# Performance work log

Measured on AMD Instinct MI355X. Metric: run time of the kernel, lower is better.

The kernel has to match this reference:

```python
import jax, jax.numpy as jnp
import numpy as np

IMG_H, IMG_W = 432.0, 768.0
B, N = 8, 1_000_000


def setup_inputs() -> dict:
    key = jax.random.key(0)
    k1, k2 = jax.random.split(key)
    scores = jax.random.uniform(k1, (B, N, 1), dtype=jnp.float32)
    # center-format boxes (x, y, w, h) roughly in image coords so masks fire
    scale = jnp.array([IMG_W, IMG_H, 256.0, 256.0], dtype=jnp.float32)
    rps = jax.random.uniform(k2, (B, N, 4), dtype=jnp.float32) * scale
    return {"scores": scores, "rps": rps, "n_train_pre_nms": 12000}


def _anchors_clip(boxes):
    # boxes: [B, N, 4] in (cx, cy, w, h)
    cx, cy, w, h = boxes[..., 0], boxes[..., 1], boxes[..., 2], boxes[..., 3]
    x1 = jnp.clip(cx - w * 0.5, 0.0, IMG_W)
    x2 = jnp.clip(cx + w * 0.5, 0.0, IMG_W)
    y1 = jnp.clip(cy - h * 0.5, 0.0, IMG_H)
    y2 = jnp.clip(cy + h * 0.5, 0.0, IMG_H)
    nw = x2 - x1
    nh = y2 - y1
    nx = x1 + nw * 0.5
    ny = y1 + nh * 0.5
    return jnp.stack([nx, ny, nw, nh], axis=-1)


def reference(scores, rps, n_train_pre_nms):
    rois = _anchors_clip(rps)                                   # [B, N, 4]
    mask = ((rois[..., 2] > 16.0) & (rois[..., 3] > 16.0))
    s = scores * mask.astype(scores.dtype)[..., None]           # [B, N, 1]
    # full descending argsort along anchor dim, keep top n_train_pre_nms
    order = jnp.argsort(-s[..., 0], axis=1)[:, :n_train_pre_nms]  # [B, K]
    rois_sel = jnp.take_along_axis(rois, order[..., None], axis=1)  # [B, K, 4]
    s_sel = jnp.take_along_axis(s, order[..., None], axis=1)        # [B, K, 1]
    return rois_sel, s_sel
```

## Files before the change

kernel.cpp:

```cpp
#include <hip/hip_runtime.h>
#include <stdint.h>

#define BATCH   8
#define NITEMS  1000000
#define NC      64
#define NF      4096
#define NBLK    128
#define CAP     32768
#define TOPBIN  (NC - 1)
#define IMG_W   768.0f
#define IMG_H   432.0f

static __device__ __forceinline__ float clip0(float v, float hi) {
    return fminf(fmaxf(v, 0.0f), hi);
}
static __device__ __forceinline__ int cbin(float s) {
    int g = (int)(s * (float)NC);
    return g > NC - 1 ? NC - 1 : (g < 0 ? 0 : g);
}
static __device__ __forceinline__ int fbin(float s, int g) {
    int f = (int)(s * (float)(NC * NF)) - g * NF;
    return f > NF - 1 ? NF - 1 : (f < 0 ? 0 : f);
}
static __device__ __forceinline__ unsigned mkbits(float4 box, float s) {
    float x1 = clip0(box.x - box.z * 0.5f, IMG_W);
    float x2 = clip0(box.x + box.z * 0.5f, IMG_W);
    float y1 = clip0(box.y - box.w * 0.5f, IMG_H);
    float y2 = clip0(box.y + box.w * 0.5f, IMG_H);
    bool m = ((x2 - x1) > 16.0f) && ((y2 - y1) > 16.0f);
    return __float_as_uint(m ? s : 0.0f);
}

__global__ __launch_bounds__(512)
void k_bits_hist(const float* __restrict__ scores,
                 const float4* __restrict__ rps,
                 uint4* __restrict__ bits_arr,
                 unsigned short* __restrict__ p1,
                 unsigned short* __restrict__ p2) {
    __shared__ unsigned h1[NC];
    __shared__ unsigned h2[NF];
    const int b = blockIdx.y, blk = blockIdx.x, tid = threadIdx.x;
    if (tid < NC) h1[tid] = 0u;
    for (int k = tid; k < NF; k += 512) h2[k] = 0u;
    __syncthreads();
    const int base = b * NITEMS;
    for (int i0 = (blk * 512 + tid) * 4; i0 < NITEMS; i0 += NBLK * 512 * 4) {
        const float4 sc = *(const float4*)(scores + base + i0);
        const float4 bx0 = rps[base + i0 + 0];
        const float4 bx1 = rps[base + i0 + 1];
        const float4 bx2 = rps[base + i0 + 2];
        const float4 bx3 = rps[base + i0 + 3];
        uint4 ob;
        ob.x = mkbits(bx0, sc.x);
        ob.y = mkbits(bx1, sc.y);
        ob.z = mkbits(bx2, sc.z);
        ob.w = mkbits(bx3, sc.w);
        unsigned arr[4] = {ob.x, ob.y, ob.z, ob.w};
        #pragma unroll
        for (int j = 0; j < 4; j++) {
            unsigned bits = arr[j];
            if (bits) {
                float s = __uint_as_float(bits);
                int g = cbin(s);
                atomicAdd(&h1[g], 1u);
                if (g == TOPBIN) atomicAdd(&h2[fbin(s, TOPBIN)], 1u);
            }
        }
        bits_arr[(base + i0) >> 2] = ob;
    }
    __syncthreads();
    const size_t row1 = (size_t)(b * NBLK + blk) * NC;
    if (tid < NC) p1[row1 + tid] = (unsigned short)h1[tid];
    const size_t row2 = (size_t)(b * NBLK + blk) * NF;
    for (int k = tid; k < NF; k += 512) p2[row2 + k] = (unsigned short)h2[k];
}

__global__ __launch_bounds__(256)
void k_scan1(const unsigned short* __restrict__ p1,
             unsigned* __restrict__ chist64,
             unsigned* __restrict__ csuf64,
             unsigned* __restrict__ ctrA,
             unsigned* __restrict__ meta,
             int K) {
    const int b = blockIdx.x, tid = threadIdx.x;
    __shared__ unsigned sm[256];
    const int bin = tid & (NC - 1);
    const int chunk = tid >> 6;
    unsigned s = 0;
    for (int k = chunk * 32; k < chunk * 32 + 32; k++)
        s += p1[(size_t)(b * NBLK + k) * NC + bin];
    sm[tid] = s;
    __syncthreads();
    if (tid < NC)
        sm[tid] = sm[tid] + sm[64 + tid] + sm[128 + tid] + sm[192 + tid];
    __syncthreads();
    if (tid == 0) {
        unsigned run = 0, cbb = 0, nAb = 0;
        bool found = false;
        for (int g = NC - 1; g >= 0; g--) {
            unsigned c = sm[g];
            chist64[b * NC + g] = c;
            csuf64[b * NC + g] = run;
            if (!found && run < (unsigned)K && run + c >= (unsigned)K) {
                cbb = (unsigned)g; nAb = run; found = true;
            }
            run += c;
        }
        meta[b * 4 + 0] = cbb;
        meta[b * 4 + 1] = nAb;
    }
    if (tid < NC) ctrA[b * NC + tid] = 0u;
}

__global__ __launch_bounds__(512)
void k_fine_fb(const unsigned* __restrict__ bits_arr,
               const unsigned* __restrict__ meta,
               unsigned short* __restrict__ p2) {
    const int b = blockIdx.y, blk = blockIdx.x, tid = threadIdx.x;
    const unsigned cbb = meta[b * 4 + 0];
    if (cbb == TOPBIN) return;
    __shared__ unsigned h2[NF];
    for (int k = tid; k < NF; k += 512) h2[k] = 0u;
    __syncthreads();
    const int base = b * NITEMS;
    for (int i = blk * 512 + tid; i < NITEMS; i += NBLK * 512) {
        unsigned bits = bits_arr[base + i];
        if (!bits) continue;
        float s = __uint_as_float(bits);
        if ((unsigned)cbin(s) == cbb) atomicAdd(&h2[fbin(s, (int)cbb)], 1u);
    }
    __syncthreads();
    const size_t row = (size_t)(b * NBLK + blk) * NF;
    for (int k = tid; k < NF; k += 512) p2[row + k] = (unsigned short)h2[k];
}

__global__ __launch_bounds__(1024)
void k_scan2(const unsigned short* __restrict__ p2,
             unsigned* __restrict__ fhist,
             unsigned* __restrict__ fsuf,
             unsigned* __restrict__ ctrB,
             unsigned* __restrict__ meta,
             int K) {
    const int b = blockIdx.x, tid = threadIdx.x;
    __shared__ unsigned sc[1024];
    const int binbase = 4 * (1023 - tid);
    unsigned a0 = 0, a1 = 0, a2 = 0, a3 = 0;
    for (int k = 0; k < NBLK; k++) {
        const ushort4 v = *(const ushort4*)(p2 + (size_t)(b * NBLK + k) * NF + binbase);
        a0 += v.x; a1 += v.y; a2 += v.z; a3 += v.w;
    }
    unsigned cw[4] = {a3, a2, a1, a0};
    unsigned pin[4];
    unsigned run = 0;
    #pragma unroll
    for (int k = 0; k < 4; k++) { run += cw[k]; pin[k] = run; }
    sc[tid] = run;
    __syncthreads();
    unsigned x = run;
    for (int off = 1; off < 1024; off <<= 1) {
        unsigned t = (tid >= off) ? sc[tid - off] : 0u;
        __syncthreads();
        x += t;
        sc[tid] = x;
        __syncthreads();
    }
    const unsigned exclBase = x - run;
    const unsigned nAb = meta[b * 4 + 1];
    #pragma unroll
    for (int k = 0; k < 4; k++) {
        int g = binbase + (3 - k);
        unsigned excl = exclBase + pin[k] - cw[k];
        fsuf[b * NF + g] = excl;
        fhist[b * NF + g] = cw[k];
        unsigned t0 = nAb + excl;
        if (t0 < (unsigned)K && t0 + cw[k] >= (unsigned)K) {
            meta[b * 4 + 2] = (unsigned)g;
            meta[b * 4 + 3] = t0 + cw[k];
        }
    }
    if (tid == 0 && nAb + sc[1023] < (unsigned)K) {
        meta[b * 4 + 2] = 0u;
        meta[b * 4 + 3] = nAb + sc[1023];
    }
    ctrB[b * NF + tid * 4 + 0] = 0u;
    ctrB[b * NF + tid * 4 + 1] = 0u;
    ctrB[b * NF + tid * 4 + 2] = 0u;
    ctrB[b * NF + tid * 4 + 3] = 0u;
}

__global__ __launch_bounds__(512)
void k_compact(const uint4* __restrict__ bits_arr,
               const unsigned* __restrict__ meta,
               const unsigned* __restrict__ csuf64,
               const unsigned* __restrict__ fsuf,
               unsigned* __restrict__ ctrA,
               unsigned* __restrict__ ctrB,
               unsigned long long* __restrict__ cand) {
    const int b = blockIdx.y;
    const unsigned cbb = meta[b * 4 + 0];
    const unsigned nAb = meta[b * 4 + 1];
    const unsigned fb  = meta[b * 4 + 2];
    const int base = b * NITEMS;
    for (int i0 = (blockIdx.x * 512 + threadIdx.x) * 4; i0 < NITEMS;
         i0 += NBLK * 512 * 4) {
        uint4 v = bits_arr[(base + i0) >> 2];
        unsigned arr[4] = {v.x, v.y, v.z, v.w};
        #pragma unroll
        for (int j = 0; j < 4; j++) {
            unsigned bits = arr[j];
            if (!bits) continue;
            float s = __uint_as_float(bits);
            int g = cbin(s);
            if ((unsigned)g < cbb) continue;
            unsigned slot;
            if ((unsigned)g > cbb) {
                slot = csuf64[b * NC + g] + atomicAdd(&ctrA[b * NC + g], 1u);
            } else {
                int f = fbin(s, g);
                if ((unsigned)f < fb) continue;
                slot = nAb + fsuf[b * NF + f] + atomicAdd(&ctrB[b * NF + f], 1u);
            }
            if (slot < CAP)
                cand[(size_t)b * CAP + slot] =
                    ((unsigned long long)bits << 32) | (unsigned)(~(unsigned)(i0 + j));
        }
    }
}

__global__ __launch_bounds__(256)
void k_rank_out(const unsigned long long* __restrict__ cand,
                const unsigned* __restrict__ meta,
                const unsigned* __restrict__ csuf64,
                const unsigned* __restrict__ chist64,
                const unsigned* __restrict__ fsuf,
                const unsigned* __restrict__ fhist,
                const float4* __restrict__ rps,
                float* __restrict__ out,
                int K) {
    const int b = blockIdx.y;
    unsigned total = meta[b * 4 + 3];
    if (total > CAP) total = CAP;
    const unsigned p = blockIdx.x * 256 + threadIdx.x;
    if (p >= total) return;
    const unsigned long long key = cand[(size_t)b * CAP + p];
    const unsigned bits = (unsigned)(key >> 32);
    const float s = __uint_as_float(bits);
    const unsigned cbb = meta[b * 4 + 0];
    const unsigned nAb = meta[b * 4 + 1];
    int g = cbin(s);
    unsigned sbase, scnt;
    if ((unsigned)g > cbb) {
        sbase = csuf64[b * NC + g];
        scnt  = chist64[b * NC + g];
    } else {
        int f = fbin(s, g);
        sbase = nAb + fsuf[b * NF + f];
        scnt  = fhist[b * NF + f];
    }
    unsigned send = sbase + scnt;
    if (send > total) send = total;
    unsigned rank = sbase;
    for (unsigned j = sbase; j < send; j++)
        rank += (cand[(size_t)b * CAP + j] > key) ? 1u : 0u;
    if (rank < (unsigned)K) {
        unsigned idx = ~((unsigned)key);
        float4 box = rps[(size_t)b * NITEMS + idx];
        float x1 = clip0(box.x - box.z * 0.5f, IMG_W);
        float x2 = clip0(box.x + box.z * 0.5f, IMG_W);
        float y1 = clip0(box.y - box.w * 0.5f, IMG_H);
        float y2 = clip0(box.y + box.w * 0.5f, IMG_H);
        float nw = x2 - x1, nh = y2 - y1;
        float nx = x1 + nw * 0.5f, ny = y1 + nh * 0.5f;
        ((float4*)out)[(size_t)b * K + rank] = make_float4(nx, ny, nw, nh);
        out[(size_t)BATCH * K * 4 + (size_t)b * K + rank] = s;
    }
}

extern "C" void kernel_launch(void* const* d_in, const int* in_sizes, int n_in,
                              void* d_out, int out_size, void* d_ws, size_t ws_size,
                              hipStream_t stream) {
    const float*  scores = (const float*)d_in[0];
    const float4* rps    = (const float4*)d_in[1];
    const int K = out_size / (BATCH * 5);

    uint8_t* w = (uint8_t*)d_ws;
    uint4* bits_arr          = (uint4*)(w);
    unsigned short* p1       = (unsigned short*)(w + 32000000);
    unsigned short* p2       = (unsigned short*)(w + 32200000);
    unsigned* chist64        = (unsigned*)(w + 40600000);
    unsigned* csuf64         = (unsigned*)(w + 40610000);
    unsigned* fhist          = (unsigned*)(w + 40700000);
    unsigned* fsuf           = (unsigned*)(w + 40900000);
    unsigned* ctrA           = (unsigned*)(w + 41100000);
    unsigned* ctrB           = (unsigned*)(w + 41200000);
    unsigned* meta           = (unsigned*)(w + 41400000);
    unsigned long long* cand = (unsigned long long*)(w + 41500000);

    k_bits_hist<<<dim3(NBLK, BATCH), dim3(512), 0, stream>>>(scores, rps, bits_arr, p1, p2);
    k_scan1<<<dim3(BATCH), dim3(256), 0, stream>>>(p1, chist64, csuf64, ctrA, meta, K);
    k_fine_fb<<<dim3(NBLK, BATCH), dim3(512), 0, stream>>>((const unsigned*)bits_arr, meta, p2);
    k_scan2<<<dim3(BATCH), dim3(1024), 0, stream>>>(p2, fhist, fsuf, ctrB, meta, K);
    k_compact<<<dim3(NBLK, BATCH), dim3(512), 0, stream>>>(bits_arr, meta, csuf64, fsuf,
                                                           ctrA, ctrB, cand);
    k_rank_out<<<dim3(CAP / 256, BATCH), dim3(256), 0, stream>>>(cand, meta, csuf64, chist64,
                                                                 fsuf, fhist, rps,
                                                                 (float*)d_out, K);
}
```

Baseline: 84.91 us.

## Double histogram grid, privatize coarse bins per wave, add parallel fine-histogram reduce

```diff
diff --git a/kernel.cpp b/kernel.cpp
--- a/kernel.cpp
+++ b/kernel.cpp
@@ -1,15 +1,18 @@
 #include <hip/hip_runtime.h>
 #include <stdint.h>
 
-#define BATCH   8
-#define NITEMS  1000000
-#define NC      64
-#define NF      4096
-#define NBLK    128
-#define CAP     32768
-#define TOPBIN  (NC - 1)
-#define IMG_W   768.0f
-#define IMG_H   432.0f
+#define BATCH    8
+#define NITEMS   1000000
+#define NC       64
+#define NF       4096
+#define NBLKA    256
+#define NBLKF    128
+#define CAP      32768
+#define TOPBIN   (NC - 1)
+#define IMG_W    768.0f
+#define IMG_H    432.0f
+
+typedef unsigned long long ull;
 
 static __device__ __forceinline__ float clip0(float v, float hi) {
     return fminf(fmaxf(v, 0.0f), hi);
@@ -31,48 +34,64 @@
     return __float_as_uint(m ? s : 0.0f);
 }
 
-__global__ __launch_bounds__(512)
-void k_bits_hist(const float* __restrict__ scores,
-                 const float4* __restrict__ rps,
-                 uint4* __restrict__ bits_arr,
-                 unsigned short* __restrict__ p1,
-                 unsigned short* __restrict__ p2) {
-    __shared__ unsigned h1[NC];
+__global__ __launch_bounds__(256, 4)
+void k_bits(const float* __restrict__ scores,
+            const float4* __restrict__ rps,
+            uint4* __restrict__ bits_arr,
+            unsigned short* __restrict__ p1,
+            unsigned short* __restrict__ p2) {
+    __shared__ unsigned h1[4][NC];
     __shared__ unsigned h2[NF];
     const int b = blockIdx.y, blk = blockIdx.x, tid = threadIdx.x;
-    if (tid < NC) h1[tid] = 0u;
-    for (int k = tid; k < NF; k += 512) h2[k] = 0u;
-    __syncthreads();
-    const int base = b * NITEMS;
-    for (int i0 = (blk * 512 + tid) * 4; i0 < NITEMS; i0 += NBLK * 512 * 4) {
-        const float4 sc = *(const float4*)(scores + base + i0);
-        const float4 bx0 = rps[base + i0 + 0];
-        const float4 bx1 = rps[base + i0 + 1];
-        const float4 bx2 = rps[base + i0 + 2];
-        const float4 bx3 = rps[base + i0 + 3];
-        uint4 ob;
-        ob.x = mkbits(bx0, sc.x);
-        ob.y = mkbits(bx1, sc.y);
-        ob.z = mkbits(bx2, sc.z);
-        ob.w = mkbits(bx3, sc.w);
-        unsigned arr[4] = {ob.x, ob.y, ob.z, ob.w};
+    const int wave = tid >> 6;
+    for (int k = tid; k < NF; k += 256) h2[k] = 0u;
+    if (tid < NC) {
+        h1[0][tid] = 0u; h1[1][tid] = 0u; h1[2][tid] = 0u; h1[3][tid] = 0u;
+    }
+    __syncthreads();
+    const size_t base = (size_t)b * NITEMS;
+    const float4* sp = (const float4*)(scores + base);
+    const float4* rp = rps + base;
+    for (int i0 = (blk * 256 + tid) * 8; i0 < NITEMS; i0 += NBLKA * 256 * 8) {
+        const int q = i0 >> 2;
+        const float4 s0 = sp[q];
+        const float4 s1 = sp[q + 1];
+        const float4 b0 = rp[i0 + 0];
+        const float4 b1 = rp[i0 + 1];
+        const float4 b2 = rp[i0 + 2];
+        const float4 b3 = rp[i0 + 3];
+        const float4 b4 = rp[i0 + 4];
+        const float4 b5 = rp[i0 + 5];
+        const float4 b6 = rp[i0 + 6];
+        const float4 b7 = rp[i0 + 7];
+        unsigned arr[8];
+        arr[0] = mkbits(b0, s0.x);
+        arr[1] = mkbits(b1, s0.y);
+        arr[2] = mkbits(b2, s0.z);
+        arr[3] = mkbits(b3, s0.w);
+        arr[4] = mkbits(b4, s1.x);
+        arr[5] = mkbits(b5, s1.y);
+        arr[6] = mkbits(b6, s1.z);
+        arr[7] = mkbits(b7, s1.w);
+        bits_arr[(base >> 2) + q]     = make_uint4(arr[0], arr[1], arr[2], arr[3]);
+        bits_arr[(base >> 2) + q + 1] = make_uint4(arr[4], arr[5], arr[6], arr[7]);
         #pragma unroll
-        for (int j = 0; j < 4; j++) {
+        for (int j = 0; j < 8; ++j) {
             unsigned bits = arr[j];
             if (bits) {
                 float s = __uint_as_float(bits);
                 int g = cbin(s);
-                atomicAdd(&h1[g], 1u);
+                atomicAdd(&h1[wave][g], 1u);
                 if (g == TOPBIN) atomicAdd(&h2[fbin(s, TOPBIN)], 1u);
             }
         }
-        bits_arr[(base + i0) >> 2] = ob;
-    }
-    __syncthreads();
-    const size_t row1 = (size_t)(b * NBLK + blk) * NC;
-    if (tid < NC) p1[row1 + tid] = (unsigned short)h1[tid];
-    const size_t row2 = (size_t)(b * NBLK + blk) * NF;
-    for (int k = tid; k < NF; k += 512) p2[row2 + k] = (unsigned short)h2[k];
+    }
+    __syncthreads();
+    if (tid < NC)
+        p1[(size_t)(b * NBLKA + blk) * NC + tid] =
+            (unsigned short)(h1[0][tid] + h1[1][tid] + h1[2][tid] + h1[3][tid]);
+    const size_t row2 = (size_t)(b * NBLKA + blk) * NF;
+    for (int k = tid; k < NF; k += 256) p2[row2 + k] = (unsigned short)h2[k];
 }
 
 __global__ __launch_bounds__(256)
@@ -84,20 +103,18 @@
              int K) {
     const int b = blockIdx.x, tid = threadIdx.x;
     __shared__ unsigned sm[256];
-    const int bin = tid & (NC - 1);
-    const int chunk = tid >> 6;
+    const int bin = tid & 63, chunk = tid >> 6;
     unsigned s = 0;
-    for (int k = chunk * 32; k < chunk * 32 + 32; k++)
-        s += p1[(size_t)(b * NBLK + k) * NC + bin];
+    for (int k = chunk * 64; k < chunk * 64 + 64; ++k)
+        s += p1[(size_t)(b * NBLKA + k) * NC + bin];
     sm[tid] = s;
     __syncthreads();
-    if (tid < NC)
-        sm[tid] = sm[tid] + sm[64 + tid] + sm[128 + tid] + sm[192 + tid];
+    if (tid < NC) sm[tid] = sm[tid] + sm[64 + tid] + sm[128 + tid] + sm[192 + tid];
     __syncthreads();
     if (tid == 0) {
         unsigned run = 0, cbb = 0, nAb = 0;
         bool found = false;
-        for (int g = NC - 1; g >= 0; g--) {
+        for (int g = NC - 1; g >= 0; --g) {
             unsigned c = sm[g];
             chist64[b * NC + g] = c;
             csuf64[b * NC + g] = run;
@@ -112,30 +129,41 @@
     if (tid < NC) ctrA[b * NC + tid] = 0u;
 }
 
-__global__ __launch_bounds__(512)
-void k_fine_fb(const unsigned* __restrict__ bits_arr,
+__global__ __launch_bounds__(256)
+void k_fine_fb(const unsigned* __restrict__ bits_lin,
                const unsigned* __restrict__ meta,
                unsigned short* __restrict__ p2) {
     const int b = blockIdx.y, blk = blockIdx.x, tid = threadIdx.x;
     const unsigned cbb = meta[b * 4 + 0];
     if (cbb == TOPBIN) return;
     __shared__ unsigned h2[NF];
-    for (int k = tid; k < NF; k += 512) h2[k] = 0u;
+    for (int k = tid; k < NF; k += 256) h2[k] = 0u;
     __syncthreads();
     const int base = b * NITEMS;
-    for (int i = blk * 512 + tid; i < NITEMS; i += NBLK * 512) {
-        unsigned bits = bits_arr[base + i];
+    for (int i = blk * 256 + tid; i < NITEMS; i += NBLKA * 256) {
+        unsigned bits = bits_lin[base + i];
         if (!bits) continue;
         float s = __uint_as_float(bits);
         if ((unsigned)cbin(s) == cbb) atomicAdd(&h2[fbin(s, (int)cbb)], 1u);
     }
     __syncthreads();
-    const size_t row = (size_t)(b * NBLK + blk) * NF;
-    for (int k = tid; k < NF; k += 512) p2[row + k] = (unsigned short)h2[k];
+    const size_t row = (size_t)(b * NBLKA + blk) * NF;
+    for (int k = tid; k < NF; k += 256) p2[row + k] = (unsigned short)h2[k];
+}
+
+__global__ __launch_bounds__(256)
+void k_reduce_fine(const unsigned short* __restrict__ p2,
+                   unsigned* __restrict__ red2) {
+    const int b = blockIdx.y;
+    const int g = blockIdx.x * 256 + threadIdx.x;
+    const unsigned short* p = p2 + (size_t)b * NBLKA * NF + g;
+    unsigned s = 0;
+    for (int k = 0; k < NBLKA; ++k) s += p[(size_t)k * NF];
+    red2[b * NF + g] = s;
 }
 
 __global__ __launch_bounds__(1024)
-void k_scan2(const unsigned short* __restrict__ p2,
+void k_scan2(const unsigned* __restrict__ red2,
              unsigned* __restrict__ fhist,
              unsigned* __restrict__ fsuf,
              unsigned* __restrict__ ctrB,
@@ -144,12 +172,8 @@
     const int b = blockIdx.x, tid = threadIdx.x;
     __shared__ unsigned sc[1024];
     const int binbase = 4 * (1023 - tid);
-    unsigned a0 = 0, a1 = 0, a2 = 0, a3 = 0;
-    for (int k = 0; k < NBLK; k++) {
-        const ushort4 v = *(const ushort4*)(p2 + (size_t)(b * NBLK + k) * NF + binbase);
-        a0 += v.x; a1 += v.y; a2 += v.z; a3 += v.w;
-    }
-    unsigned cw[4] = {a3, a2, a1, a0};
+    const uint4 v = *(const uint4*)(red2 + b * NF + binbase);
+    unsigned cw[4] = {v.w, v.z, v.y, v.x};
     unsigned pin[4];
     unsigned run = 0;
     #pragma unroll
@@ -195,14 +219,14 @@
                const unsigned* __restrict__ fsuf,
                unsigned* __restrict__ ctrA,
                unsigned* __restrict__ ctrB,
-               unsigned long long* __restrict__ cand) {
+               ull* __restrict__ cand) {
     const int b = blockIdx.y;
     const unsigned cbb = meta[b * 4 + 0];
     const unsigned nAb = meta[b * 4 + 1];
     const unsigned fb  = meta[b * 4 + 2];
     const int base = b * NITEMS;
     for (int i0 = (blockIdx.x * 512 + threadIdx.x) * 4; i0 < NITEMS;
-         i0 += NBLK * 512 * 4) {
+         i0 += NBLKF * 512 * 4) {
         uint4 v = bits_arr[(base + i0) >> 2];
         unsigned arr[4] = {v.x, v.y, v.z, v.w};
         #pragma unroll
@@ -222,13 +246,13 @@
             }
             if (slot < CAP)
                 cand[(size_t)b * CAP + slot] =
-                    ((unsigned long long)bits << 32) | (unsigned)(~(unsigned)(i0 + j));
+                    ((ull)bits << 32) | (unsigned)(~(unsigned)(i0 + j));
         }
     }
 }
 
 __global__ __launch_bounds__(256)
-void k_rank_out(const unsigned long long* __restrict__ cand,
+void k_rank_out(const ull* __restrict__ cand,
                 const unsigned* __restrict__ meta,
                 const unsigned* __restrict__ csuf64,
                 const unsigned* __restrict__ chist64,
@@ -242,7 +266,7 @@
     if (total > CAP) total = CAP;
     const unsigned p = blockIdx.x * 256 + threadIdx.x;
     if (p >= total) return;
-    const unsigned long long key = cand[(size_t)b * CAP + p];
+    const ull key = cand[(size_t)b * CAP + p];
     const unsigned bits = (unsigned)(key >> 32);
     const float s = __uint_as_float(bits);
     const unsigned cbb = meta[b * 4 + 0];
@@ -284,25 +308,28 @@
     const int K = out_size / (BATCH * 5);
 
     uint8_t* w = (uint8_t*)d_ws;
-    uint4* bits_arr          = (uint4*)(w);
-    unsigned short* p1       = (unsigned short*)(w + 32000000);
-    unsigned short* p2       = (unsigned short*)(w + 32200000);
-    unsigned* chist64        = (unsigned*)(w + 40600000);
-    unsigned* csuf64         = (unsigned*)(w + 40610000);
-    unsigned* fhist          = (unsigned*)(w + 40700000);
-    unsigned* fsuf           = (unsigned*)(w + 40900000);
-    unsigned* ctrA           = (unsigned*)(w + 41100000);
-    unsigned* ctrB           = (unsigned*)(w + 41200000);
-    unsigned* meta           = (unsigned*)(w + 41400000);
-    unsigned long long* cand = (unsigned long long*)(w + 41500000);
-
-    k_bits_hist<<<dim3(NBLK, BATCH), dim3(512), 0, stream>>>(scores, rps, bits_arr, p1, p2);
+    uint4* bits_arr     = (uint4*)(w);
+    unsigned short* p1  = (unsigned short*)(w + 32000000);
+    unsigned short* p2  = (unsigned short*)(w + 32300000);
+    unsigned* red2      = (unsigned*)(w + 49100000);
+    unsigned* chist64   = (unsigned*)(w + 49240000);
+    unsigned* csuf64    = (unsigned*)(w + 49250000);
+    unsigned* fhist     = (unsigned*)(w + 49260000);
+    unsigned* fsuf      = (unsigned*)(w + 49400000);
+    unsigned* ctrA      = (unsigned*)(w + 49540000);
+    unsigned* ctrB      = (unsigned*)(w + 49550000);
+    unsigned* meta      = (unsigned*)(w + 49690000);
+    ull* cand           = (ull*)(w + 49700000);
+
+    k_bits<<<dim3(NBLKA, BATCH), dim3(256), 0, stream>>>(scores, rps, bits_arr, p1, p2);
     k_scan1<<<dim3(BATCH), dim3(256), 0, stream>>>(p1, chist64, csuf64, ctrA, meta, K);
-    k_fine_fb<<<dim3(NBLK, BATCH), dim3(512), 0, stream>>>((const unsigned*)bits_arr, meta, p2);
-    k_scan2<<<dim3(BATCH), dim3(1024), 0, stream>>>(p2, fhist, fsuf, ctrB, meta, K);
-    k_compact<<<dim3(NBLK, BATCH), dim3(512), 0, stream>>>(bits_arr, meta, csuf64, fsuf,
-                                                           ctrA, ctrB, cand);
-    k_rank_out<<<dim3(CAP / 256, BATCH), dim3(256), 0, stream>>>(cand, meta, csuf64, chist64,
-                                                                 fsuf, fhist, rps,
-                                                                 (float*)d_out, K);
-}
+    k_fine_fb<<<dim3(NBLKA, BATCH), dim3(256), 0, stream>>>((const unsigned*)bits_arr,
+                                                            meta, p2);
+    k_reduce_fine<<<dim3(NF / 256, BATCH), dim3(256), 0, stream>>>(p2, red2);
+    k_scan2<<<dim3(BATCH), dim3(1024), 0, stream>>>(red2, fhist, fsuf, ctrB, meta, K);
+    k_compact<<<dim3(NBLKF, BATCH), dim3(512), 0, stream>>>(bits_arr, meta, csuf64, fsuf,
+                                                            ctrA, ctrB, cand);
+    k_rank_out<<<dim3(CAP / 256, BATCH), dim3(256), 0, stream>>>(cand, meta, csuf64,
+                                                                 chist64, fsuf, fhist,
+                                                                 rps, (float*)d_out, K);
+}
```

Measured after the change: 87.28 us. 1.03x slower.
